# Optimization experiments

Hardware: AMD Instinct MI355X
Metric: run time of the kernel (lower is better)

Reference implementation:

```python
import jax, jax.numpy as jnp
import numpy as np

OUT_H = 7
OUT_W = 7
SPATIAL_SCALE = 0.25
SAMPLING_RATIO = 2  # exact sampling branch (sampling_ratio > 0)
ALIGNED = True


def setup_inputs() -> dict:
    key = jax.random.key(0)
    k1, k2, k3, k4 = jax.random.split(key, 4)
    feat = jax.random.normal(k1, (4, 256, 100, 100), dtype=jnp.float32)
    # rois[K,5]: (batch_idx, x1, y1, x2, y2) in image coords (image ~400px since scale=0.25)
    K = 512
    bidx = jax.random.randint(k2, (K,), 0, 4).astype(jnp.float32)
    xy1 = jax.random.uniform(k3, (K, 2), minval=0.0, maxval=300.0, dtype=jnp.float32)
    wh = jax.random.uniform(k4, (K, 2), minval=20.0, maxval=99.0, dtype=jnp.float32)
    xy2 = xy1 + wh
    rois = jnp.concatenate([bidx[:, None], xy1[:, 0:1], xy1[:, 1:2], xy2[:, 0:1], xy2[:, 1:2]], axis=1)
    return {"input": feat, "rois": rois}


def _roi_align(feat, rois):
    N, C, H, W = feat.shape
    b = rois[:, 0].astype(jnp.int32)  # [K]
    offset = 0.5 if ALIGNED else 0.0
    sw = rois[:, 1] * SPATIAL_SCALE - offset
    sh = rois[:, 2] * SPATIAL_SCALE - offset
    ew = rois[:, 3] * SPATIAL_SCALE - offset
    eh = rois[:, 4] * SPATIAL_SCALE - offset
    rw = ew - sw
    rh = eh - sh
    if not ALIGNED:
        rw = jnp.maximum(rw, 1.0)
        rh = jnp.maximum(rh, 1.0)
    bin_h = rh / OUT_H  # [K]
    bin_w = rw / OUT_W

    ph = jnp.arange(OUT_H, dtype=feat.dtype)
    pw = jnp.arange(OUT_W, dtype=feat.dtype)
    samp = jnp.arange(SAMPLING_RATIO, dtype=feat.dtype) + 0.5  # (i + 0.5)

    # y: [K, OUT_H, SR], x: [K, OUT_W, SR]
    y = sh[:, None, None] + ph[None, :, None] * bin_h[:, None, None] + samp[None, None, :] * (bin_h / SAMPLING_RATIO)[:, None, None]
    x = sw[:, None, None] + pw[None, :, None] * bin_w[:, None, None] + samp[None, None, :] * (bin_w / SAMPLING_RATIO)[:, None, None]

    # bilinear interpolation indices/weights (matches _bilinear_interpolate)
    y = jnp.maximum(y, 0.0)
    x = jnp.maximum(x, 0.0)
    yl = y.astype(jnp.int32)
    xl = x.astype(jnp.int32)
    yh = jnp.where(yl >= H - 1, H - 1, yl + 1)
    yl = jnp.where(yl >= H - 1, H - 1, yl)
    xh = jnp.where(xl >= W - 1, W - 1, xl + 1)
    xl = jnp.where(xl >= W - 1, W - 1, xl)
    ly = y - yl.astype(feat.dtype)
    lx = x - xl.astype(feat.dtype)
    hy = 1.0 - ly
    hx = 1.0 - lx

    def gather(yi, xi):
        # yi: [K,PH,IY], xi: [K,PW,IX] -> [K,PH,IY,PW,IX,C]
        return feat[b[:, None, None, None, None], :,
                    yi[:, :, :, None, None],
                    xi[:, None, None, :, :]]

    v1 = gather(yl, xl)
    v2 = gather(yl, xh)
    v3 = gather(yh, xl)
    v4 = gather(yh, xh)

    out = (jnp.einsum('kpi,kqj,kpiqjc->kcpq', hy, hx, v1)
           + jnp.einsum('kpi,kqj,kpiqjc->kcpq', hy, lx, v2)
           + jnp.einsum('kpi,kqj,kpiqjc->kcpq', ly, hx, v3)
           + jnp.einsum('kpi,kqj,kpiqjc->kcpq', ly, lx, v4))
    count = float(max(SAMPLING_RATIO * SAMPLING_RATIO, 1))
    return out / count  # [K, C, OUT_H, OUT_W]


def reference(input, rois):
    return _roi_align(input, rois)
```

## Files before the change

### kernel.cpp

```cpp
#include <hip/hip_runtime.h>


#define FEAT_C 256
#define FEAT_H 100
#define FEAT_W 100
#define HW     (FEAT_H * FEAT_W)
#define NROI   512
#define NBINS  49
#define CPB    8
#define GROUPS 32
#define SCALE  0.25f
#define PROWS  25
#define PSTR   28
#define CSTR   (PSTR * PROWS)

typedef float f32x2 __attribute__((ext_vector_type(2)));

__device__ __forceinline__ void samp_geo(float s, float bsz, int idx, int sr_i,
                                         int& lo, float& fr) {
    float v = s + bsz * ((float)idx + ((float)sr_i + 0.5f) * 0.5f);
    v = fmaxf(v, 0.0f);
    int l = (int)v;
    if (l > FEAT_H - 1) l = FEAT_H - 1;
    fr = v - (float)l;
    lo = l;
}

__global__ __launch_bounds__(256) void roialign_fwd(
    const float* __restrict__ feat,
    const float* __restrict__ rois,
    float* __restrict__ out)
{
    __shared__ __align__(16) float s_patch[CPB * CSTR];
    __shared__ __align__(16) int2  s_yg[14];
    __shared__ __align__(16) int2  s_xg[14];
    __shared__ __align__(16) int   s_meta[8];

    const int bid = blockIdx.x;
    const int k   = bid >> 5;
    const int cg  = bid & (GROUPS - 1);
    const int tid = threadIdx.x;

    if (tid < 32) {
        const float* r = rois + k * 5;
        if (tid == 28) s_meta[0] = (int)r[0];
        if (tid < 28) {
            const bool isy = tid < 14;
            const int  t   = isy ? tid : tid - 14;
            float s   = (isy ? r[2] : r[1]) * SCALE - 0.5f;
            float e   = (isy ? r[4] : r[3]) * SCALE - 0.5f;
            float bsz = (e - s) * (1.0f / 7.0f);
            int lo; float fr;
            samp_geo(s, bsz, t >> 1, t & 1, lo, fr);
            int o0; float fd;
            samp_geo(s, bsz, 0, 0, o0, fd);
            if (isy) {
                s_yg[t] = make_int2((lo - o0) * PSTR, __float_as_int(fr));
                if (t == 13) { s_meta[1] = o0; s_meta[3] = lo - o0 + 2; }
            } else {
                int a0 = o0 & ~3;
                if (lo >= FEAT_W - 1) fr = 0.0f;
                s_xg[t] = make_int2(lo - a0, __float_as_int(fr));
                if (t == 13) { s_meta[2] = a0; s_meta[4] = lo - a0 + 2; }
            }
        }
    }
    __syncthreads();

    {
        const int4 m     = *reinterpret_cast<const int4*>(s_meta);
        const int  aspan = s_meta[4];
        const int  py    = (tid * 9363) >> 16;
        const int  q     = tid - py * 7;
        if (py < m.w && q * 4 < aspan) {
            int qs = m.z + q * 4;
            if (qs > FEAT_W - 4) qs = FEAT_W - 4;
            int sy = m.y + py;
            if (sy > FEAT_H - 1) sy = FEAT_H - 1;
            const float* src = feat + ((size_t)(m.x * FEAT_C) + cg * CPB) * HW
                             + sy * FEAT_W + qs;
            float* dst = s_patch + py * PSTR + q * 4;
            #pragma unroll
            for (int c = 0; c < CPB; c++)
                *reinterpret_cast<float4*>(dst + c * CSTR) =
                    *reinterpret_cast<const float4*>(src + c * HW);
        }
    }
    __syncthreads();

    if (tid < 4 * NBINS) {
        const int cp  = (tid * 335) >> 14;
        const int bin = tid - cp * NBINS;
        const int ph  = (bin * 37) >> 8;
        const int pw  = bin - ph * 7;

        const int4 yg = *reinterpret_cast<const int4*>(&s_yg[2 * ph]);
        const int4 xg = *reinterpret_cast<const int4*>(&s_xg[2 * pw]);
        const float* pA = s_patch + (cp * 2) * CSTR;
        const float* pB = pA + CSTR;

        const float ly0 = __int_as_float(yg.y), hy0 = 1.0f - ly0;
        const float ly1 = __int_as_float(yg.w), hy1 = 1.0f - ly1;
        const float lx0 = __int_as_float(xg.y), hx0 = 1.0f - lx0;
        const float lx1 = __int_as_float(xg.w), hx1 = 1.0f - lx1;

        f32x2 acc = {0.0f, 0.0f};
        auto quad = [&](int ro, float hy, float ly, int xo, float hx, float lx) {
            const float* a = pA + ro + xo;
            const float* q = pB + ro + xo;
            f32x2 vL0 = {a[0],        q[0]};
            f32x2 vL1 = {a[1],        q[1]};
            f32x2 vH0 = {a[PSTR],     q[PSTR]};
            f32x2 vH1 = {a[PSTR + 1], q[PSTR + 1]};
            f32x2 t = vL0 * hx + vL1 * lx;
            f32x2 u = vH0 * hx + vH1 * lx;
            acc += t * hy + u * ly;
        };
        quad(yg.x, hy0, ly0, xg.x, hx0, lx0);
        quad(yg.x, hy0, ly0, xg.z, hx1, lx1);
        quad(yg.z, hy1, ly1, xg.x, hx0, lx0);
        quad(yg.z, hy1, ly1, xg.z, hx1, lx1);
        acc *= 0.25f;

        float* ob = out + ((size_t)k * FEAT_C + cg * CPB + cp * 2) * NBINS + bin;
        ob[0]     = acc.x;
        ob[NBINS] = acc.y;
    }
}

extern "C" void kernel_launch(void* const* d_in, const int* in_sizes, int n_in,
                              void* d_out, int out_size, void* d_ws, size_t ws_size,
                              hipStream_t stream) {
    const float* feat = (const float*)d_in[0];
    const float* rois = (const float*)d_in[1];
    float*       outp = (float*)d_out;
    roialign_fwd<<<dim3(NROI * GROUPS), dim3(256), 0, stream>>>(feat, rois, outp);
}
```

Baseline: 104.6 us.

## Make each wavefront an independent ROI/channel-pair worker without block barriers

Each 64-lane wavefront now handles one ROI and two channels on its own, with a private LDS slice and its own geometry table. The table is built with readlane, so no block-wide __syncthreads or shared metadata is needed. This removes block synchronisation and idle threads. The trade-off is that ROI geometry is recomputed per wave and fewer channels share one patch load. Launch bounds now ask for 6 blocks per CU.

```diff
diff --git a/kernel.cpp b/kernel.cpp
--- a/kernel.cpp
+++ b/kernel.cpp
@@ -1,103 +1,96 @@
 #include <hip/hip_runtime.h>
 
 
+#define NROI   512
 #define FEAT_C 256
 #define FEAT_H 100
 #define FEAT_W 100
-#define HW     (FEAT_H * FEAT_W)
-#define NROI   512
+#define HW     10000
 #define NBINS  49
-#define CPB    8
-#define GROUPS 32
-#define SCALE  0.25f
 #define PROWS  25
 #define PSTR   28
 #define CSTR   (PSTR * PROWS)
+#define WLDS   (2 * CSTR + 56)
 
 typedef float f32x2 __attribute__((ext_vector_type(2)));
 
-__device__ __forceinline__ void samp_geo(float s, float bsz, int idx, int sr_i,
-                                         int& lo, float& fr) {
-    float v = s + bsz * ((float)idx + ((float)sr_i + 0.5f) * 0.5f);
-    v = fmaxf(v, 0.0f);
-    int l = (int)v;
-    if (l > FEAT_H - 1) l = FEAT_H - 1;
-    fr = v - (float)l;
-    lo = l;
-}
-
-__global__ __launch_bounds__(256) void roialign_fwd(
+__global__ __launch_bounds__(256, 6) void roialign_fwd(
     const float* __restrict__ feat,
     const float* __restrict__ rois,
     float* __restrict__ out)
 {
-    __shared__ __align__(16) float s_patch[CPB * CSTR];
-    __shared__ __align__(16) int2  s_yg[14];
-    __shared__ __align__(16) int2  s_xg[14];
-    __shared__ __align__(16) int   s_meta[8];
+    __shared__ __align__(16) float s_lds[4 * WLDS];
 
-    const int bid = blockIdx.x;
-    const int k   = bid >> 5;
-    const int cg  = bid & (GROUPS - 1);
-    const int tid = threadIdx.x;
+    const int tid  = threadIdx.x;
+    const int lane = tid & 63;
+    const int w    = __builtin_amdgcn_readfirstlane(tid >> 6);
+    const int W    = blockIdx.x * 4 + w;
+    const int k    = W >> 7;
+    const int cg   = W & 127;
 
-    if (tid < 32) {
-        const float* r = rois + k * 5;
-        if (tid == 28) s_meta[0] = (int)r[0];
-        if (tid < 28) {
-            const bool isy = tid < 14;
-            const int  t   = isy ? tid : tid - 14;
-            float s   = (isy ? r[2] : r[1]) * SCALE - 0.5f;
-            float e   = (isy ? r[4] : r[3]) * SCALE - 0.5f;
-            float bsz = (e - s) * (1.0f / 7.0f);
-            int lo; float fr;
-            samp_geo(s, bsz, t >> 1, t & 1, lo, fr);
-            int o0; float fd;
-            samp_geo(s, bsz, 0, 0, o0, fd);
-            if (isy) {
-                s_yg[t] = make_int2((lo - o0) * PSTR, __float_as_int(fr));
-                if (t == 13) { s_meta[1] = o0; s_meta[3] = lo - o0 + 2; }
-            } else {
-                int a0 = o0 & ~3;
-                if (lo >= FEAT_W - 1) fr = 0.0f;
-                s_xg[t] = make_int2(lo - a0, __float_as_int(fr));
-                if (t == 13) { s_meta[2] = a0; s_meta[4] = lo - a0 + 2; }
+    float* wp  = s_lds + w * WLDS;
+    int2*  tbl = (int2*)(wp + 2 * CSTR);
+
+    const float* r = rois + k * 5;
+    const float r0 = r[0], r1 = r[1], r2 = r[2], r3 = r[3], r4 = r[4];
+    const int   b  = (int)r0;
+
+    const int  t   = lane < 28 ? lane : 0;
+    const bool isy = t < 14;
+    const int  u   = isy ? t : t - 14;
+    float s   = (isy ? r2 : r1) * 0.25f - 0.5f;
+    float e   = (isy ? r4 : r3) * 0.25f - 0.5f;
+    float bsz = (e - s) * (1.0f / 7.0f);
+    float v   = s + bsz * ((float)(u >> 1) + ((float)(u & 1) + 0.5f) * 0.5f);
+    v = fmaxf(v, 0.0f);
+    int lo = (int)v;
+    if (lo > FEAT_H - 1) lo = FEAT_H - 1;
+    float fr = v - (float)lo;
+
+    const int y0  = __builtin_amdgcn_readlane(lo, 0);
+    const int yM  = __builtin_amdgcn_readlane(lo, 13);
+    const int x0  = __builtin_amdgcn_readlane(lo, 14);
+    const int xM  = __builtin_amdgcn_readlane(lo, 27);
+    const int ax0   = x0 & ~3;
+    const int rows  = yM - y0 + 2;
+    const int aspan = xM - ax0 + 2;
+
+    if (lane < 28) {
+        if (!isy && lo >= FEAT_W - 1) fr = 0.0f;
+        int off = isy ? (lo - y0) * PSTR : (lo - ax0);
+        tbl[lane] = make_int2(off, __float_as_int(fr));
+    }
+
+    const float* fb  = feat + (size_t)(b * FEAT_C + cg * 2) * HW;
+    const int row = (lane * 9363) >> 16;
+    const int q   = lane - row * 7;
+    int col = ax0 + q * 4;
+    if (col > FEAT_W - 4) col = FEAT_W - 4;
+    const bool qok = (q * 4) < aspan;
+    #pragma unroll
+    for (int c = 0; c < 2; c++) {
+        #pragma unroll
+        for (int rb = 0; rb < 3; rb++) {
+            int py = rb * 9 + row;
+            if (qok && py < rows) {
+                int sy = y0 + py;
+                if (sy > FEAT_H - 1) sy = FEAT_H - 1;
+                const float4* g = (const float4*)(fb + c * HW + sy * FEAT_W + col);
+                *(float4*)(wp + c * CSTR + py * PSTR + q * 4) = *g;
             }
         }
     }
-    __syncthreads();
 
-    {
-        const int4 m     = *reinterpret_cast<const int4*>(s_meta);
-        const int  aspan = s_meta[4];
-        const int  py    = (tid * 9363) >> 16;
-        const int  q     = tid - py * 7;
-        if (py < m.w && q * 4 < aspan) {
-            int qs = m.z + q * 4;
-            if (qs > FEAT_W - 4) qs = FEAT_W - 4;
-            int sy = m.y + py;
-            if (sy > FEAT_H - 1) sy = FEAT_H - 1;
-            const float* src = feat + ((size_t)(m.x * FEAT_C) + cg * CPB) * HW
-                             + sy * FEAT_W + qs;
-            float* dst = s_patch + py * PSTR + q * 4;
-            #pragma unroll
-            for (int c = 0; c < CPB; c++)
-                *reinterpret_cast<float4*>(dst + c * CSTR) =
-                    *reinterpret_cast<const float4*>(src + c * HW);
-        }
-    }
-    __syncthreads();
+    __builtin_amdgcn_wave_barrier();
 
-    if (tid < 4 * NBINS) {
-        const int cp  = (tid * 335) >> 14;
-        const int bin = tid - cp * NBINS;
-        const int ph  = (bin * 37) >> 8;
-        const int pw  = bin - ph * 7;
+    if (lane < NBINS) {
+        const int ph = (lane * 37) >> 8;
+        const int pw = lane - ph * 7;
 
-        const int4 yg = *reinterpret_cast<const int4*>(&s_yg[2 * ph]);
-        const int4 xg = *reinterpret_cast<const int4*>(&s_xg[2 * pw]);
-        const float* pA = s_patch + (cp * 2) * CSTR;
-        const float* pB = pA + CSTR;
+        const int4 yg = *(const int4*)(tbl + 2 * ph);
+        const int4 xg = *(const int4*)(tbl + 14 + 2 * pw);
+        const float* pA = wp;
+        const float* pB = wp + CSTR;
 
         const float ly0 = __int_as_float(yg.y), hy0 = 1.0f - ly0;
         const float ly1 = __int_as_float(yg.w), hy1 = 1.0f - ly1;
@@ -107,14 +100,14 @@
         f32x2 acc = {0.0f, 0.0f};
         auto quad = [&](int ro, float hy, float ly, int xo, float hx, float lx) {
             const float* a = pA + ro + xo;
-            const float* q = pB + ro + xo;
-            f32x2 vL0 = {a[0],        q[0]};
-            f32x2 vL1 = {a[1],        q[1]};
-            f32x2 vH0 = {a[PSTR],     q[PSTR]};
-            f32x2 vH1 = {a[PSTR + 1], q[PSTR + 1]};
-            f32x2 t = vL0 * hx + vL1 * lx;
-            f32x2 u = vH0 * hx + vH1 * lx;
-            acc += t * hy + u * ly;
+            const float* p = pB + ro + xo;
+            f32x2 vL0 = {a[0],        p[0]};
+            f32x2 vL1 = {a[1],        p[1]};
+            f32x2 vH0 = {a[PSTR],     p[PSTR]};
+            f32x2 vH1 = {a[PSTR + 1], p[PSTR + 1]};
+            f32x2 tt = vL0 * hx + vL1 * lx;
+            f32x2 uu = vH0 * hx + vH1 * lx;
+            acc += tt * hy + uu * ly;
         };
         quad(yg.x, hy0, ly0, xg.x, hx0, lx0);
         quad(yg.x, hy0, ly0, xg.z, hx1, lx1);
@@ -122,7 +115,7 @@
         quad(yg.z, hy1, ly1, xg.z, hx1, lx1);
         acc *= 0.25f;
 
-        float* ob = out + ((size_t)k * FEAT_C + cg * CPB + cp * 2) * NBINS + bin;
+        float* ob = out + ((size_t)k * FEAT_C + cg * 2) * NBINS + lane;
         ob[0]     = acc.x;
         ob[NBINS] = acc.y;
     }
@@ -134,5 +127,5 @@
     const float* feat = (const float*)d_in[0];
     const float* rois = (const float*)d_in[1];
     float*       outp = (float*)d_out;
-    roialign_fwd<<<dim3(NROI * GROUPS), dim3(256), 0, stream>>>(feat, rois, outp);
+    roialign_fwd<<<dim3(NROI * 128 / 4), dim3(256), 0, stream>>>(feat, rois, outp);
 }
```

Result: slower. 111.6 us (+6.7%).

## Fuse y-interpolation into global load, store per-sample rows in LDS

Applied to the files above, without the earlier changes.

Each thread now computes the ROI geometry itself, dropping the first barrier. During the global load it does the vertical interpolation, loading the low and high feature rows and storing one blended row per y-sample, with channel pairs interleaved in LDS. The compute phase then only does horizontal interpolation using 64-bit paired LDS reads, and launch bounds request higher occupancy. In exchange, feature rows shared between neighbouring y-samples may be loaded twice from global memory.

```diff
diff --git a/kernel.cpp b/kernel.cpp
--- a/kernel.cpp
+++ b/kernel.cpp
@@ -4,15 +4,15 @@
 #define FEAT_C 256
 #define FEAT_H 100
 #define FEAT_W 100
-#define HW     (FEAT_H * FEAT_W)
+#define HW     10000
 #define NROI   512
 #define NBINS  49
 #define CPB    8
 #define GROUPS 32
-#define SCALE  0.25f
-#define PROWS  25
-#define PSTR   28
-#define CSTR   (PSTR * PROWS)
+#define NPAIR  4
+#define YS     14
+#define RSTR   60
+#define PAIRSTR (YS * RSTR)
 
 typedef float f32x2 __attribute__((ext_vector_type(2)));
 
@@ -26,64 +26,73 @@
     lo = l;
 }
 
-__global__ __launch_bounds__(256) void roialign_fwd(
+__global__ __launch_bounds__(256, 8) void roialign_fwd(
     const float* __restrict__ feat,
     const float* __restrict__ rois,
     float* __restrict__ out)
 {
-    __shared__ __align__(16) float s_patch[CPB * CSTR];
-    __shared__ __align__(16) int2  s_yg[14];
-    __shared__ __align__(16) int2  s_xg[14];
-    __shared__ __align__(16) int   s_meta[8];
+    __shared__ __align__(16) float s_rows[NPAIR * PAIRSTR];
+    __shared__ __align__(16) int2  s_xt[YS];
 
     const int bid = blockIdx.x;
     const int k   = bid >> 5;
     const int cg  = bid & (GROUPS - 1);
     const int tid = threadIdx.x;
 
-    if (tid < 32) {
-        const float* r = rois + k * 5;
-        if (tid == 28) s_meta[0] = (int)r[0];
-        if (tid < 28) {
-            const bool isy = tid < 14;
-            const int  t   = isy ? tid : tid - 14;
-            float s   = (isy ? r[2] : r[1]) * SCALE - 0.5f;
-            float e   = (isy ? r[4] : r[3]) * SCALE - 0.5f;
-            float bsz = (e - s) * (1.0f / 7.0f);
-            int lo; float fr;
-            samp_geo(s, bsz, t >> 1, t & 1, lo, fr);
-            int o0; float fd;
-            samp_geo(s, bsz, 0, 0, o0, fd);
-            if (isy) {
-                s_yg[t] = make_int2((lo - o0) * PSTR, __float_as_int(fr));
-                if (t == 13) { s_meta[1] = o0; s_meta[3] = lo - o0 + 2; }
-            } else {
-                int a0 = o0 & ~3;
-                if (lo >= FEAT_W - 1) fr = 0.0f;
-                s_xg[t] = make_int2(lo - a0, __float_as_int(fr));
-                if (t == 13) { s_meta[2] = a0; s_meta[4] = lo - a0 + 2; }
-            }
-        }
+    const float* r = rois + k * 5;
+    const int   b  = (int)r[0];
+    const float sw = r[1] * 0.25f - 0.5f;
+    const float sh = r[2] * 0.25f - 0.5f;
+    const float ew = r[3] * 0.25f - 0.5f;
+    const float eh = r[4] * 0.25f - 0.5f;
+    const float bh = (eh - sh) * (1.0f / 7.0f);
+    const float bw = (ew - sw) * (1.0f / 7.0f);
+
+    int x0; float fd;
+    samp_geo(sw, bw, 0, 0, x0, fd);
+    const int ax0 = x0 & ~3;
+
+    if (tid < YS) {
+        int lo; float fr;
+        samp_geo(sw, bw, tid >> 1, tid & 1, lo, fr);
+        if (lo >= FEAT_W - 1) fr = 0.0f;
+        s_xt[tid] = make_int2((lo - ax0) * 2, __float_as_int(fr));
     }
-    __syncthreads();
 
-    {
-        const int4 m     = *reinterpret_cast<const int4*>(s_meta);
-        const int  aspan = s_meta[4];
-        const int  py    = (tid * 9363) >> 16;
-        const int  q     = tid - py * 7;
-        if (py < m.w && q * 4 < aspan) {
-            int qs = m.z + q * 4;
-            if (qs > FEAT_W - 4) qs = FEAT_W - 4;
-            int sy = m.y + py;
-            if (sy > FEAT_H - 1) sy = FEAT_H - 1;
-            const float* src = feat + ((size_t)(m.x * FEAT_C) + cg * CPB) * HW
-                             + sy * FEAT_W + qs;
-            float* dst = s_patch + py * PSTR + q * 4;
-            #pragma unroll
-            for (int c = 0; c < CPB; c++)
-                *reinterpret_cast<float4*>(dst + c * CSTR) =
-                    *reinterpret_cast<const float4*>(src + c * HW);
+    if (tid < 2 * 98) {
+        const int half = tid >= 98;
+        const int sid  = tid - 98 * half;
+        const int ys   = (sid * 9363) >> 16;
+        const int q    = sid - ys * 7;
+
+        int yl; float fry;
+        samp_geo(sh, bh, ys >> 1, ys & 1, yl, fry);
+        int yh = yl + 1; if (yh > FEAT_H - 1) yh = FEAT_H - 1;
+        const float hyw = 1.0f - fry, lyw = fry;
+
+        int col = ax0 + q * 4;
+        if (col > FEAT_W - 4) col = FEAT_W - 4;
+
+        const float* fb = feat + (size_t)(b * FEAT_C + cg * CPB) * HW
+                        + yl * FEAT_W + col;
+        const int dyh = (yh - yl) * FEAT_W;
+        float* dbase = s_rows + ys * RSTR + q * 8;
+
+        for (int p = 2 * half; p < 2 * half + 2; p++) {
+            const float* c0 = fb + (2 * p) * HW;
+            const float* c1 = c0 + HW;
+            float4 L0 = *(const float4*)(c0);
+            float4 H0 = *(const float4*)(c0 + dyh);
+            float4 L1 = *(const float4*)(c1);
+            float4 H1 = *(const float4*)(c1 + dyh);
+            float4 r0, r1;
+            r0.x = L0.x * hyw + H0.x * lyw;  r0.y = L0.y * hyw + H0.y * lyw;
+            r0.z = L0.z * hyw + H0.z * lyw;  r0.w = L0.w * hyw + H0.w * lyw;
+            r1.x = L1.x * hyw + H1.x * lyw;  r1.y = L1.y * hyw + H1.y * lyw;
+            r1.z = L1.z * hyw + H1.z * lyw;  r1.w = L1.w * hyw + H1.w * lyw;
+            float* d = dbase + p * PAIRSTR;
+            *(float4*)(d)     = make_float4(r0.x, r1.x, r0.y, r1.y);
+            *(float4*)(d + 4) = make_float4(r0.z, r1.z, r0.w, r1.w);
         }
     }
     __syncthreads();
@@ -94,32 +103,22 @@
         const int ph  = (bin * 37) >> 8;
         const int pw  = bin - ph * 7;
 
-        const int4 yg = *reinterpret_cast<const int4*>(&s_yg[2 * ph]);
-        const int4 xg = *reinterpret_cast<const int4*>(&s_xg[2 * pw]);
-        const float* pA = s_patch + (cp * 2) * CSTR;
-        const float* pB = pA + CSTR;
-
-        const float ly0 = __int_as_float(yg.y), hy0 = 1.0f - ly0;
-        const float ly1 = __int_as_float(yg.w), hy1 = 1.0f - ly1;
+        const int4 xg = *(const int4*)(&s_xt[2 * pw]);
         const float lx0 = __int_as_float(xg.y), hx0 = 1.0f - lx0;
         const float lx1 = __int_as_float(xg.w), hx1 = 1.0f - lx1;
 
+        const float* P = s_rows + cp * PAIRSTR + (2 * ph) * RSTR;
         f32x2 acc = {0.0f, 0.0f};
-        auto quad = [&](int ro, float hy, float ly, int xo, float hx, float lx) {
-            const float* a = pA + ro + xo;
-            const float* q = pB + ro + xo;
-            f32x2 vL0 = {a[0],        q[0]};
-            f32x2 vL1 = {a[1],        q[1]};
-            f32x2 vH0 = {a[PSTR],     q[PSTR]};
-            f32x2 vH1 = {a[PSTR + 1], q[PSTR + 1]};
-            f32x2 t = vL0 * hx + vL1 * lx;
-            f32x2 u = vH0 * hx + vH1 * lx;
-            acc += t * hy + u * ly;
-        };
-        quad(yg.x, hy0, ly0, xg.x, hx0, lx0);
-        quad(yg.x, hy0, ly0, xg.z, hx1, lx1);
-        quad(yg.z, hy1, ly1, xg.x, hx0, lx0);
-        quad(yg.z, hy1, ly1, xg.z, hx1, lx1);
+        #pragma unroll
+        for (int iy = 0; iy < 2; iy++) {
+            const float* row = P + iy * RSTR;
+            const f32x2* A = (const f32x2*)(row + xg.x);
+            f32x2 a0 = A[0], a1 = A[1];
+            const f32x2* B = (const f32x2*)(row + xg.z);
+            f32x2 b0 = B[0], b1 = B[1];
+            acc += a0 * hx0 + a1 * lx0;
+            acc += b0 * hx1 + b1 * lx1;
+        }
         acc *= 0.25f;
 
         float* ob = out + ((size_t)k * FEAT_C + cg * CPB + cp * 2) * NBINS + bin;
```

Result: no change. 105.2 us (+0.5%).
